# Kernel tuning notes

Hardware: AMD Instinct MI355X
Metric: run time of the kernel (lower is better)

The kernel has to match this reference:

```python
import jax, jax.numpy as jnp
import numpy as np

TOP_K = 2  # num_active_experts


def setup_inputs() -> dict:
    key = jax.random.key(0)
    k1, k2, k3 = jax.random.split(key, 3)
    N, D, E = 16384, 1024, 8
    x = jax.random.normal(k1, (N, D), dtype=jnp.float32)
    router_w = jax.random.normal(k2, (E, D), dtype=jnp.float32) * (1.0 / np.sqrt(D))
    router_b = jnp.zeros((E,), dtype=jnp.float32)
    expert_w = jax.random.normal(k3, (E, D, D), dtype=jnp.float32) * (1.0 / np.sqrt(D))
    expert_b = jnp.zeros((E, D), dtype=jnp.float32)
    return {"x": x, "router_w": router_w, "router_b": router_b,
            "expert_w": expert_w, "expert_b": expert_b}


def reference(x, router_w, router_b, expert_w, expert_b):
    E = router_w.shape[0]
    # Router: softmax over experts, pick top-k, renormalize
    logits = x @ router_w.T + router_b                      # [N, E]
    probs = jax.nn.softmax(logits, axis=-1)                 # [N, E]
    top_p, top_i = jax.lax.top_k(probs, TOP_K)              # [N, K]
    top_p = top_p / jnp.sum(top_p, axis=-1, keepdims=True)  # renormalized gates
    # Dense combine weights: [N, E], zero for non-selected experts
    combine = jnp.sum(jax.nn.one_hot(top_i, E, dtype=x.dtype) * top_p[..., None], axis=1)
    # All-expert outputs, then weighted combine (vectorized dispatch/combine)
    y = jnp.einsum('nd,eod->neo', x, expert_w) + expert_b   # [N, E, O]
    out = jnp.einsum('neo,ne->no', y, combine)              # [N, O]
    return out
```

## Files before the change

kernel.cpp:

```cpp
#include <hip/hip_runtime.h>
#include <hip/hip_bf16.h>


constexpr int DIMS = 1024;
constexpr int NE   = 8;
constexpr int ROUTER_BLOCKS = 1024;
constexpr int WCONV_BLOCKS  = NE * DIMS * DIMS / (8 * 256);
constexpr int RT_PER_XCD = 33;

typedef __attribute__((ext_vector_type(8))) short short8;
typedef __attribute__((ext_vector_type(4))) short short4_t;
typedef __attribute__((ext_vector_type(4))) float f32x4;

typedef const __attribute__((address_space(1))) void* gp_t;
typedef __attribute__((address_space(3))) void* sp_t;

__device__ __forceinline__ float b2f(unsigned short u) {
  union { unsigned int i; float f; } x; x.i = ((unsigned)u) << 16; return x.f;
}
__device__ __forceinline__ short f2bs(float f) {
  __hip_bfloat16 h = __float2bfloat16(f);
  return *(short*)&h;
}

__global__ __launch_bounds__(256) void prep_kernel(
    const float* __restrict__ x, const float* __restrict__ rw,
    const float* __restrict__ rb, const float* __restrict__ ew,
    __hip_bfloat16* __restrict__ xb, __hip_bfloat16* __restrict__ wb,
    int* __restrict__ blk_cnt, int* __restrict__ tmp_meta,
    float* __restrict__ tmp_gate, int n_tok) {
  const int tid = threadIdx.x;

  if ((int)blockIdx.x >= ROUTER_BLOCKS) {
    unsigned g = (unsigned)(blockIdx.x - ROUTER_BLOCKS) * 256 + tid;
    int l  = g & 63;
    int kc = (g >> 6) & 31;
    int nb = (g >> 11) & 63;
    int e  = g >> 17;
    int row = nb * 16 + (l & 15);
    int kb  = kc * 32 + ((l >> 4) << 3);
    const float4* src = (const float4*)(ew + ((size_t)e << 20) + (size_t)row * DIMS + kb);
    float4 a = src[0], b = src[1];
    union { __hip_bfloat16 h[8]; float4 f; } u;
    u.h[0] = __float2bfloat16(a.x); u.h[1] = __float2bfloat16(a.y);
    u.h[2] = __float2bfloat16(a.z); u.h[3] = __float2bfloat16(a.w);
    u.h[4] = __float2bfloat16(b.x); u.h[5] = __float2bfloat16(b.y);
    u.h[6] = __float2bfloat16(b.z); u.h[7] = __float2bfloat16(b.w);
    ((float4*)wb)[g] = u.f;
    return;
  }

  __shared__ float s_rw[NE * DIMS];
  __shared__ int s_cnt[NE];
  __shared__ int s_e[32];
  __shared__ float s_g[32];
  __shared__ int s_pos[32];

  const float4* rw4g = (const float4*)rw;
  float4* s4 = (float4*)s_rw;
  for (int i = tid; i < NE * DIMS / 4; i += 256) s4[i] = rw4g[i];
  if (tid < NE) s_cnt[tid] = 0;
  __syncthreads();

  const float4* s_rw4 = (const float4*)s_rw;
  const int wave = tid >> 6, lane = tid & 63;
  for (int i = 0; i < 4; ++i) {
    int t = blockIdx.x * 16 + wave * 4 + i;
    const float4* xr = (const float4*)(x + (size_t)t * DIMS);
    short4_t* xw = (short4_t*)(xb + (size_t)t * DIMS);
    float a[NE];
#pragma unroll
    for (int e = 0; e < NE; ++e) a[e] = 0.f;
#pragma unroll
    for (int j = 0; j < 4; ++j) {
      float4 v = xr[lane + j * 64];
      short4_t p;
      p[0] = f2bs(v.x); p[1] = f2bs(v.y); p[2] = f2bs(v.z); p[3] = f2bs(v.w);
      xw[lane + j * 64] = p;
#pragma unroll
      for (int e = 0; e < NE; ++e) {
        float4 w = s_rw4[e * 256 + lane + j * 64];
        a[e] = fmaf(v.x, w.x, fmaf(v.y, w.y, fmaf(v.z, w.z, fmaf(v.w, w.w, a[e]))));
      }
    }
#pragma unroll
    for (int off = 32; off > 0; off >>= 1) {
#pragma unroll
      for (int e = 0; e < NE; ++e) a[e] += __shfl_xor(a[e], off, 64);
    }
    if (lane == 0) {
      float l[NE];
#pragma unroll
      for (int e = 0; e < NE; ++e) l[e] = a[e] + rb[e];
      int e0 = 0;
#pragma unroll
      for (int e = 1; e < NE; ++e) if (l[e] > l[e0]) e0 = e;
      int e1 = (e0 == 0) ? 1 : 0;
#pragma unroll
      for (int e = 0; e < NE; ++e) if (e != e0 && l[e] > l[e1]) e1 = e;
      float r = expf(l[e1] - l[e0]);
      float g0 = 1.f / (1.f + r);
      float g1 = 1.f - g0;
      int ai = (wave * 4 + i) * 2;
      int p0 = atomicAdd(&s_cnt[e0], 1);
      int p1 = atomicAdd(&s_cnt[e1], 1);
      s_e[ai] = e0; s_g[ai] = g0; s_pos[ai] = p0;
      s_e[ai + 1] = e1; s_g[ai + 1] = g1; s_pos[ai + 1] = p1;
    }
  }
  __syncthreads();
  if (tid < NE) blk_cnt[blockIdx.x * NE + tid] = s_cnt[tid];
  if (tid < 32) {
    int s = blockIdx.x * 32 + tid;
    tmp_meta[s] = s_e[tid] | (s_pos[tid] << 3);
    tmp_gate[s] = s_g[tid];
  }
}

__global__ __launch_bounds__(512) void scan_kernel(
    const int* __restrict__ blk_cnt, int* __restrict__ blk_base,
    int* __restrict__ counts) {
  const int e = threadIdx.x >> 6, lane = threadIdx.x & 63;
  int running = 0;
  for (int c = 0; c < ROUTER_BLOCKS / 64; ++c) {
    int v = blk_cnt[(c * 64 + lane) * NE + e];
    int incl = v;
#pragma unroll
    for (int off = 1; off < 64; off <<= 1) {
      int t = __shfl_up(incl, off, 64);
      if (lane >= off) incl += t;
    }
    blk_base[(c * 64 + lane) * NE + e] = running + incl - v;
    running += __shfl(incl, 63, 64);
  }
  if (lane == 0) counts[e] = running;
}

__global__ __launch_bounds__(256) void scatter_kernel(
    const int* __restrict__ tmp_meta, const float* __restrict__ tmp_gate,
    const int* __restrict__ blk_base, int* __restrict__ entries,
    float* __restrict__ gates, int n_tok) {
  int s = blockIdx.x * 256 + threadIdx.x;
  int meta = tmp_meta[s];
  int e = meta & 7, pos = meta >> 3;
  int p = blk_base[(s >> 5) * NE + e] + pos;
  entries[e * n_tok + p] = ((s >> 1) << 1) | (s & 1);
  gates[e * n_tok + p] = tmp_gate[s];
}

__global__ __launch_bounds__(256, 4) void moe_gemm(
    const __hip_bfloat16* __restrict__ xb, const __hip_bfloat16* __restrict__ wb,
    const float* __restrict__ eb, const int* __restrict__ counts,
    const int* __restrict__ entries, const float* __restrict__ gates,
    __hip_bfloat16* __restrict__ y, int n_tok) {
  const int xcd = blockIdx.x & 7;
  const int j = blockIdx.x >> 3;
  const int ct = j & 7;
  const int virt = xcd * RT_PER_XCD + (j >> 3);

  int e = -1, rt = 0, cnt = 0, acc_t = 0;
#pragma unroll
  for (int i = 0; i < NE; ++i) {
    int c = counts[i];
    int t = (c + 127) >> 7;
    if (e < 0 && virt < acc_t + t) { e = i; rt = virt - acc_t; cnt = c; }
    acc_t += t;
  }
  if (e < 0) return;

  __shared__ __hip_bfloat16 As[128 * 32];

  const int tid = threadIdx.x;
  const int lane = tid & 63, wave = tid >> 6;
  const int row0 = rt * 128;
  const int n0 = ct * 128;

  const int srow = tid >> 2;
  const int kcs = (tid & 3) ^ (srow & 3);
  const int kcol = kcs * 8;
  int gr0 = row0 + srow, gr1 = row0 + srow + 64;
  int ent0 = (gr0 < cnt) ? entries[e * n_tok + gr0] : 0;
  int ent1 = (gr1 < cnt) ? entries[e * n_tok + gr1] : 0;
  const __hip_bfloat16* ap0 = xb + (size_t)(ent0 >> 1) * DIMS + kcol;
  const __hip_bfloat16* ap1 = xb + (size_t)(ent1 >> 1) * DIMS + kcol;

  const int wm = (wave & 1) * 64, wn = (wave >> 1) * 64;
  const int fr = lane & 15, quad = lane >> 4;
  const int swo = (quad ^ (fr & 3)) * 8;

  const short8* wb8 = (const short8*)wb;
  const size_t bbase = (((size_t)e * 64 + ((n0 + wn) >> 4)) * 32) * 64 + lane;

  f32x4 acc[4][4] = {};

  for (int ks = 0; ks < 32; ++ks) {
    __builtin_amdgcn_global_load_lds((gp_t)(ap0 + ks * 32), (sp_t)(As + tid * 8), 16, 0, 0);
    __builtin_amdgcn_global_load_lds((gp_t)(ap1 + ks * 32), (sp_t)(As + (tid + 256) * 8), 16, 0, 0);
    short8 bf[4];
#pragma unroll
    for (int nt = 0; nt < 4; ++nt)
      bf[nt] = wb8[bbase + (size_t)nt * 2048 + ks * 64];
    __syncthreads();
    short8 af[4];
#pragma unroll
    for (int mt = 0; mt < 4; ++mt)
      af[mt] = *(const short8*)&As[(wm + mt * 16 + fr) * 32 + swo];
#pragma unroll
    for (int mt = 0; mt < 4; ++mt)
#pragma unroll
      for (int nt = 0; nt < 4; ++nt)
        acc[mt][nt] = __builtin_amdgcn_mfma_f32_16x16x32_bf16(af[mt], bf[nt], acc[mt][nt], 0, 0, 0);
    __syncthreads();
  }

  float bias[4];
#pragma unroll
  for (int nt = 0; nt < 4; ++nt) bias[nt] = eb[e * DIMS + n0 + wn + nt * 16 + fr];
#pragma unroll
  for (int mt = 0; mt < 4; ++mt) {
#pragma unroll
    for (int r = 0; r < 4; ++r) {
      int m = wm + mt * 16 + quad * 4 + r;
      int gr = row0 + m;
      if (gr < cnt) {
        int ent = entries[e * n_tok + gr];
        float g = gates[e * n_tok + gr];
        __hip_bfloat16* yp = y + (size_t)ent * DIMS + n0 + wn + fr;
#pragma unroll
        for (int nt = 0; nt < 4; ++nt)
          yp[nt * 16] = __float2bfloat16(g * (acc[mt][nt][r] + bias[nt]));
      }
    }
  }
}

__global__ __launch_bounds__(256) void combine_kernel(const __hip_bfloat16* __restrict__ y,
                                                      float* __restrict__ out) {
  size_t idx = (size_t)blockIdx.x * 256 + threadIdx.x;
  size_t n = idx >> 7;
  int c = (int)(idx & 127) << 3;
  short8 v0 = *(const short8*)(y + (n * 2) * DIMS + c);
  short8 v1 = *(const short8*)(y + (n * 2 + 1) * DIMS + c);
  float4 o0, o1;
  o0.x = b2f((unsigned short)v0[0]) + b2f((unsigned short)v1[0]);
  o0.y = b2f((unsigned short)v0[1]) + b2f((unsigned short)v1[1]);
  o0.z = b2f((unsigned short)v0[2]) + b2f((unsigned short)v1[2]);
  o0.w = b2f((unsigned short)v0[3]) + b2f((unsigned short)v1[3]);
  o1.x = b2f((unsigned short)v0[4]) + b2f((unsigned short)v1[4]);
  o1.y = b2f((unsigned short)v0[5]) + b2f((unsigned short)v1[5]);
  o1.z = b2f((unsigned short)v0[6]) + b2f((unsigned short)v1[6]);
  o1.w = b2f((unsigned short)v0[7]) + b2f((unsigned short)v1[7]);
  float* op = out + n * DIMS + c;
  ((float4*)op)[0] = o0;
  ((float4*)op)[1] = o1;
}

extern "C" void kernel_launch(void* const* d_in, const int* in_sizes, int n_in,
                              void* d_out, int out_size, void* d_ws, size_t ws_size,
                              hipStream_t stream) {
  const float* x  = (const float*)d_in[0];
  const float* rw = (const float*)d_in[1];
  const float* rb = (const float*)d_in[2];
  const float* ew = (const float*)d_in[3];
  const float* eb = (const float*)d_in[4];
  float* out = (float*)d_out;
  const int n_tok = in_sizes[0] / DIMS;
  const int n_slot = 2 * n_tok;

  char* ws = (char*)d_ws;
  size_t off = 0;
  int* counts = (int*)ws;                      off += 256;
  int* blk_cnt = (int*)(ws + off);             off += (size_t)ROUTER_BLOCKS * NE * 4;
  int* blk_base = (int*)(ws + off);            off += (size_t)ROUTER_BLOCKS * NE * 4;
  int* tmp_meta = (int*)(ws + off);            off += (size_t)n_slot * 4;
  float* tmp_gate = (float*)(ws + off);        off += (size_t)n_slot * 4;
  __hip_bfloat16* xb = (__hip_bfloat16*)(ws + off); off += (size_t)n_tok * DIMS * 2;
  __hip_bfloat16* wb = (__hip_bfloat16*)(ws + off); off += (size_t)NE * DIMS * DIMS * 2;
  int*   entries = (int*)(ws + off);           off += (size_t)NE * n_tok * 4;
  float* gates   = (float*)(ws + off);         off += (size_t)NE * n_tok * 4;
  __hip_bfloat16* y = (__hip_bfloat16*)(ws + off); off += (size_t)n_slot * DIMS * 2;
  if (ws_size < off) return;

  prep_kernel<<<ROUTER_BLOCKS + WCONV_BLOCKS, 256, 0, stream>>>(
      x, rw, rb, ew, xb, wb, blk_cnt, tmp_meta, tmp_gate, n_tok);
  scan_kernel<<<1, 512, 0, stream>>>(blk_cnt, blk_base, counts);
  scatter_kernel<<<n_slot / 256, 256, 0, stream>>>(
      tmp_meta, tmp_gate, blk_base, entries, gates, n_tok);
  moe_gemm<<<8 * RT_PER_XCD * 8, 256, 0, stream>>>(
      xb, wb, eb, counts, entries, gates, y, n_tok);
  combine_kernel<<<(unsigned)((size_t)n_tok * DIMS / 8 / 256), 256, 0, stream>>>(y, out);
}
```

Baseline: 273.4 us.

## Rewrite MoE GEMM with 192x256x64 tiles, double-buffered LDS for A and B

```diff
diff --git a/kernel.cpp b/kernel.cpp
--- a/kernel.cpp
+++ b/kernel.cpp
@@ -6,7 +6,8 @@
 constexpr int NE   = 8;
 constexpr int ROUTER_BLOCKS = 1024;
 constexpr int WCONV_BLOCKS  = NE * DIMS * DIMS / (8 * 256);
-constexpr int RT_PER_XCD = 33;
+constexpr int BM = 192, BN = 256, BK = 64;
+constexpr int RT_PER_XCD = 23;
 
 typedef __attribute__((ext_vector_type(8))) short short8;
 typedef __attribute__((ext_vector_type(4))) short short4_t;
@@ -33,13 +34,7 @@
 
   if ((int)blockIdx.x >= ROUTER_BLOCKS) {
     unsigned g = (unsigned)(blockIdx.x - ROUTER_BLOCKS) * 256 + tid;
-    int l  = g & 63;
-    int kc = (g >> 6) & 31;
-    int nb = (g >> 11) & 63;
-    int e  = g >> 17;
-    int row = nb * 16 + (l & 15);
-    int kb  = kc * 32 + ((l >> 4) << 3);
-    const float4* src = (const float4*)(ew + ((size_t)e << 20) + (size_t)row * DIMS + kb);
+    const float4* src = (const float4*)(ew + (size_t)g * 8);
     float4 a = src[0], b = src[1];
     union { __hip_bfloat16 h[8]; float4 f; } u;
     u.h[0] = __float2bfloat16(a.x); u.h[1] = __float2bfloat16(a.y);
@@ -148,84 +143,134 @@
   gates[e * n_tok + p] = tmp_gate[s];
 }
 
-__global__ __launch_bounds__(256, 4) void moe_gemm(
+__global__ __launch_bounds__(512, 2) void moe_gemm(
     const __hip_bfloat16* __restrict__ xb, const __hip_bfloat16* __restrict__ wb,
     const float* __restrict__ eb, const int* __restrict__ counts,
     const int* __restrict__ entries, const float* __restrict__ gates,
     __hip_bfloat16* __restrict__ y, int n_tok) {
   const int xcd = blockIdx.x & 7;
   const int j = blockIdx.x >> 3;
-  const int ct = j & 7;
-  const int virt = xcd * RT_PER_XCD + (j >> 3);
+  const int ct = j & 3;
+  const int virt = xcd * RT_PER_XCD + (j >> 2);
 
   int e = -1, rt = 0, cnt = 0, acc_t = 0;
 #pragma unroll
   for (int i = 0; i < NE; ++i) {
     int c = counts[i];
-    int t = (c + 127) >> 7;
+    int t = (c + BM - 1) / BM;
     if (e < 0 && virt < acc_t + t) { e = i; rt = virt - acc_t; cnt = c; }
     acc_t += t;
   }
   if (e < 0) return;
 
-  __shared__ __hip_bfloat16 As[128 * 32];
+  __shared__ __align__(16) char smem[2 * 24576 + 2 * 32768];
 
   const int tid = threadIdx.x;
-  const int lane = tid & 63, wave = tid >> 6;
-  const int row0 = rt * 128;
-  const int n0 = ct * 128;
-
-  const int srow = tid >> 2;
-  const int kcs = (tid & 3) ^ (srow & 3);
-  const int kcol = kcs * 8;
-  int gr0 = row0 + srow, gr1 = row0 + srow + 64;
-  int ent0 = (gr0 < cnt) ? entries[e * n_tok + gr0] : 0;
-  int ent1 = (gr1 < cnt) ? entries[e * n_tok + gr1] : 0;
-  const __hip_bfloat16* ap0 = xb + (size_t)(ent0 >> 1) * DIMS + kcol;
-  const __hip_bfloat16* ap1 = xb + (size_t)(ent1 >> 1) * DIMS + kcol;
-
-  const int wm = (wave & 1) * 64, wn = (wave >> 1) * 64;
-  const int fr = lane & 15, quad = lane >> 4;
-  const int swo = (quad ^ (fr & 3)) * 8;
-
-  const short8* wb8 = (const short8*)wb;
-  const size_t bbase = (((size_t)e * 64 + ((n0 + wn) >> 4)) * 32) * 64 + lane;
-
-  f32x4 acc[4][4] = {};
-
-  for (int ks = 0; ks < 32; ++ks) {
-    __builtin_amdgcn_global_load_lds((gp_t)(ap0 + ks * 32), (sp_t)(As + tid * 8), 16, 0, 0);
-    __builtin_amdgcn_global_load_lds((gp_t)(ap1 + ks * 32), (sp_t)(As + (tid + 256) * 8), 16, 0, 0);
-    short8 bf[4];
-#pragma unroll
-    for (int nt = 0; nt < 4; ++nt)
-      bf[nt] = wb8[bbase + (size_t)nt * 2048 + ks * 64];
-    __syncthreads();
-    short8 af[4];
-#pragma unroll
-    for (int mt = 0; mt < 4; ++mt)
-      af[mt] = *(const short8*)&As[(wm + mt * 16 + fr) * 32 + swo];
-#pragma unroll
-    for (int mt = 0; mt < 4; ++mt)
+  const int l = tid & 63, w = tid >> 6;
+  const int row0 = rt * BM;
+  const int n0 = ct * BN;
+
+  const int qsw = (l & 7) ^ (l >> 3);
+  const __hip_bfloat16* aptr[3];
+  const __hip_bfloat16* bptr[4];
+#pragma unroll
+  for (int i = 0; i < 3; ++i) {
+    int R = (i * 8 + w) * 8 + (l >> 3);
+    int gr = row0 + R;
+    int ent = (gr < cnt) ? entries[e * n_tok + gr] : 0;
+    aptr[i] = xb + (size_t)(ent >> 1) * DIMS + qsw * 8;
+  }
+#pragma unroll
+  for (int i = 0; i < 4; ++i) {
+    int R = (i * 8 + w) * 8 + (l >> 3);
+    bptr[i] = wb + ((size_t)e << 20) + (size_t)(n0 + R) * DIMS + qsw * 8;
+  }
+
+  const int fr = l & 15, quad = l >> 4;
+  const int wr = w >> 2, wc = w & 3;
+  const int swz = (quad ^ (fr & 7)) << 4;
+  const int aoff0 = (wr * 96 + fr) * 128 + swz;
+  const int boff0 = (wc * 64 + fr) * 128 + swz;
+
+  auto stage = [&](int buf, int kt) {
+    const int koff = kt * 64;
+#pragma unroll
+    for (int i = 0; i < 3; ++i)
+      __builtin_amdgcn_global_load_lds(
+          (gp_t)(aptr[i] + koff),
+          (sp_t)(smem + buf * 24576 + (i * 8 + w) * 1024 + l * 16), 16, 0, 0);
+#pragma unroll
+    for (int i = 0; i < 4; ++i)
+      __builtin_amdgcn_global_load_lds(
+          (gp_t)(bptr[i] + koff),
+          (sp_t)(smem + 49152 + buf * 32768 + (i * 8 + w) * 1024 + l * 16), 16, 0, 0);
+  };
+
+  f32x4 acc[6][4] = {};
+
+  stage(0, 0);
+  stage(1, 1);
+  asm volatile("s_waitcnt vmcnt(7)" ::: "memory");
+  __builtin_amdgcn_s_barrier();
+
+  auto body = [&](int kt, int mode) {
+    const int cur = kt & 1;
+    const char* As = smem + cur * 24576;
+    const char* Bs = smem + 49152 + cur * 32768;
+    short8 af[6], bf[4];
+#pragma unroll
+    for (int mt = 0; mt < 6; ++mt) af[mt] = *(const short8*)(As + aoff0 + mt * 2048);
+#pragma unroll
+    for (int nt = 0; nt < 4; ++nt) bf[nt] = *(const short8*)(Bs + boff0 + nt * 2048);
+    __builtin_amdgcn_s_setprio(1);
+#pragma unroll
+    for (int mt = 0; mt < 6; ++mt)
 #pragma unroll
       for (int nt = 0; nt < 4; ++nt)
         acc[mt][nt] = __builtin_amdgcn_mfma_f32_16x16x32_bf16(af[mt], bf[nt], acc[mt][nt], 0, 0, 0);
-    __syncthreads();
-  }
+    __builtin_amdgcn_s_setprio(0);
+    short8 af2[6], bf2[4];
+#pragma unroll
+    for (int mt = 0; mt < 6; ++mt) af2[mt] = *(const short8*)(As + ((aoff0 + mt * 2048) ^ 64));
+#pragma unroll
+    for (int nt = 0; nt < 4; ++nt) bf2[nt] = *(const short8*)(Bs + ((boff0 + nt * 2048) ^ 64));
+    asm volatile("s_waitcnt lgkmcnt(0)" ::: "memory");
+    __builtin_amdgcn_s_barrier();
+    if (mode == 0) stage(cur, kt + 2);
+    __builtin_amdgcn_s_setprio(1);
+#pragma unroll
+    for (int mt = 0; mt < 6; ++mt)
+#pragma unroll
+      for (int nt = 0; nt < 4; ++nt)
+        acc[mt][nt] = __builtin_amdgcn_mfma_f32_16x16x32_bf16(af2[mt], bf2[nt], acc[mt][nt], 0, 0, 0);
+    __builtin_amdgcn_s_setprio(0);
+    if (mode == 0) {
+      asm volatile("s_waitcnt vmcnt(7)" ::: "memory");
+      __builtin_amdgcn_s_barrier();
+    } else if (mode == 1) {
+      asm volatile("s_waitcnt vmcnt(0)" ::: "memory");
+      __builtin_amdgcn_s_barrier();
+    }
+  };
+
+#pragma unroll 1
+  for (int kt = 0; kt < 14; ++kt) body(kt, 0);
+  body(14, 1);
+  body(15, 2);
 
   float bias[4];
 #pragma unroll
-  for (int nt = 0; nt < 4; ++nt) bias[nt] = eb[e * DIMS + n0 + wn + nt * 16 + fr];
-#pragma unroll
-  for (int mt = 0; mt < 4; ++mt) {
+  for (int nt = 0; nt < 4; ++nt) bias[nt] = eb[e * DIMS + n0 + wc * 64 + nt * 16 + fr];
+#pragma unroll
+  for (int mt = 0; mt < 6; ++mt) {
 #pragma unroll
     for (int r = 0; r < 4; ++r) {
-      int m = wm + mt * 16 + quad * 4 + r;
+      int m = wr * 96 + mt * 16 + quad * 4 + r;
       int gr = row0 + m;
       if (gr < cnt) {
         int ent = entries[e * n_tok + gr];
         float g = gates[e * n_tok + gr];
-        __hip_bfloat16* yp = y + (size_t)ent * DIMS + n0 + wn + fr;
+        __hip_bfloat16* yp = y + (size_t)ent * DIMS + n0 + wc * 64 + fr;
 #pragma unroll
         for (int nt = 0; nt < 4; ++nt)
           yp[nt * 16] = __float2bfloat16(g * (acc[mt][nt][r] + bias[nt]));
@@ -286,7 +331,7 @@
   scan_kernel<<<1, 512, 0, stream>>>(blk_cnt, blk_base, counts);
   scatter_kernel<<<n_slot / 256, 256, 0, stream>>>(
       tmp_meta, tmp_gate, blk_base, entries, gates, n_tok);
-  moe_gemm<<<8 * RT_PER_XCD * 8, 256, 0, stream>>>(
+  moe_gemm<<<8 * RT_PER_XCD * 4, 512, 0, stream>>>(
       xb, wb, eb, counts, entries, gates, y, n_tok);
   combine_kernel<<<(unsigned)((size_t)n_tok * DIMS / 8 / 256), 256, 0, stream>>>(y, out);
 }
```

After: 266.4 us. 1.03x faster.
